# Performance work log

Measured on AMD Instinct MI355X. Metric: run time of the kernel, lower is better.

Reference implementation:

```python
import jax, jax.numpy as jnp
import numpy as np
import math

B, L, N, DIM, H = 2, 8, 1024, 512, 8
DH = DIM // H

def setup_inputs() -> dict:
    key = jax.random.key(0)
    ks = jax.random.split(key, 9)
    s = 1.0 / math.sqrt(DIM)
    return {
        "x": jax.random.normal(ks[0], (B, L, N, DIM), dtype=jnp.float32),
        "Wq": jax.random.normal(ks[1], (DIM, DIM), dtype=jnp.float32) * s,
        "bq": jnp.zeros((DIM,), dtype=jnp.float32),
        "Wk": jax.random.normal(ks[2], (DIM, DIM), dtype=jnp.float32) * s,
        "bk": jnp.zeros((DIM,), dtype=jnp.float32),
        "Wv": jax.random.normal(ks[3], (DIM, DIM), dtype=jnp.float32) * s,
        "bv": jnp.zeros((DIM,), dtype=jnp.float32),
        "Wo": jax.random.normal(ks[4], (DIM, DIM), dtype=jnp.float32) * s,
        "bo": jnp.zeros((DIM,), dtype=jnp.float32),
    }

def _split_heads(t):
    # 'b l n (h d) -> b l h n d'
    b, l, n, _ = t.shape
    return t.reshape(b, l, n, H, DH).transpose(0, 1, 3, 2, 4)

def reference(x, Wq, bq, Wk, bk, Wv, bv, Wo, bo):
    q = _split_heads(x @ Wq.T + bq)
    # FAITHFUL BUG: source maps (q, v, k) -> (q_mat, k_mat, v_mat),
    # so the "keys" come from the v projection and "values" from the k projection.
    k_mat = _split_heads(x @ Wv.T + bv)
    v_mat = _split_heads(x @ Wk.T + bk)
    # scale is sqrt(Dh * num_heads) = sqrt(dim), as in the source
    scores = jnp.einsum('blhnd,blhmd->blhnm', q, k_mat) / math.sqrt(DIM)
    weights = jax.nn.softmax(scores, axis=-1)
    inter = jnp.einsum('blhnm,blhmd->blhnd', weights, v_mat)
    # 'b l h n d -> b l n (h d)'
    inter = inter.transpose(0, 1, 3, 2, 4).reshape(x.shape[0], x.shape[1], x.shape[2], DIM)
    return inter @ Wo.T + bo
```

## Files before the change

### kernel.cpp

```cpp
#include <hip/hip_runtime.h>
#include <stdint.h>

#define DIMC 512
#define NSEQ 1024
#define BLT  16
#define NHEAD 8
#define DHD  64
#define MTOT (BLT*NSEQ)

typedef float f32x4 __attribute__((ext_vector_type(4)));
typedef short s16x8 __attribute__((ext_vector_type(8)));
typedef short s16x4 __attribute__((ext_vector_type(4)));

__device__ __forceinline__ unsigned short f2bf(float f) {
    unsigned int u = __float_as_uint(f);
    u += 0x7fffu + ((u >> 16) & 1u);
    return (unsigned short)(u >> 16);
}
__device__ __forceinline__ float bf2f(unsigned short h) {
    return __uint_as_float(((unsigned int)h) << 16);
}

#define QSCALE (0.04419417382415922f * 1.4426950408889634f)

__device__ __forceinline__ void gll16(const void* g, void* l) {
    __builtin_amdgcn_global_load_lds(
        (const __attribute__((address_space(1))) void*)g,
        (__attribute__((address_space(3))) void*)l, 16, 0, 0);
}

__device__ __forceinline__ f32x4 mfma16_bf16(s16x4 a, s16x4 b, f32x4 c) {
#if __has_builtin(__builtin_amdgcn_mfma_f32_16x16x16bf16_1k)
    return __builtin_amdgcn_mfma_f32_16x16x16bf16_1k(a, b, c, 0, 0, 0);
#else
    asm volatile("v_mfma_f32_16x16x16_bf16 %0, %1, %2, %0"
                 : "+v"(c) : "v"(a), "v"(b));
    return c;
#endif
}

__device__ __forceinline__ s16x4 pack_bf16x4(float p0, float p1, float p2, float p3) {
    union { unsigned int u[2]; s16x4 v; } pk;
    asm("v_cvt_pk_bf16_f32 %0, %1, %2" : "=v"(pk.u[0]) : "v"(p0), "v"(p1));
    asm("v_cvt_pk_bf16_f32 %0, %1, %2" : "=v"(pk.u[1]) : "v"(p2), "v"(p3));
    return pk.v;
}

__device__ __forceinline__ bool detect_bf16(const unsigned short* x) {
    int t = threadIdx.x & 63;
    unsigned short v = x[2 * t];
    int e = (v >> 7) & 0xFF;
    unsigned long long ball = __ballot(e < 100 || e > 137);
    return __popcll(ball) < 16;
}

struct ConvArgs {
    const void* src[9];
    unsigned short* dst[9];
};

__global__ __launch_bounds__(256) void conv_kernel(ConvArgs a,
                                                   const unsigned short* __restrict__ xdet) {
    const bool isbf = detect_bf16(xdet);
    int b = blockIdx.x;
    int seg, idx;
    if (b < 4096)      { seg = 0; idx = (b * 256 + threadIdx.x) * 8; }
    else if (b < 4608) { int t = b - 4096; seg = 1 + (t >> 7);
                         idx = (((t & 127) * 256) + threadIdx.x) * 8; }
    else               { int i = threadIdx.x * 8; seg = 5 + (i >> 9); idx = i & 511; }
    const void* s = a.src[seg];
    unsigned short* d = a.dst[seg];
    if (isbf) {
        *(uint4*)(d + idx) = *(const uint4*)((const unsigned short*)s + idx);
    } else {
        float4 t0 = *(const float4*)((const float*)s + idx);
        float4 t1 = *(const float4*)((const float*)s + idx + 4);
        ushort4 v0{f2bf(t0.x), f2bf(t0.y), f2bf(t0.z), f2bf(t0.w)};
        ushort4 v1{f2bf(t1.x), f2bf(t1.y), f2bf(t1.z), f2bf(t1.w)};
        *(ushort4*)(d + idx)     = v0;
        *(ushort4*)(d + idx + 4) = v1;
    }
}

__device__ __forceinline__ void gemm_core_async(
    const unsigned short* __restrict__ Ap, const unsigned short* __restrict__ Wp,
    int mBase, int nBase, unsigned short* Al, unsigned short* Bl, f32x4 acc[4][4])
{
    const int wave = threadIdx.x >> 6;
    const int lane = threadIdx.x & 63;
    const int lr = lane & 15, lg = lane >> 4;
    const int wm = wave >> 1, wn = wave & 1;
    const int srow = lane >> 3;
    const int scol = (lane & 7) * 8;

    #pragma unroll
    for (int a = 0; a < 4; ++a)
        #pragma unroll
        for (int b = 0; b < 4; ++b) acc[a][b] = (f32x4){0.f, 0.f, 0.f, 0.f};

    for (int k0 = 0; k0 < DIMC; k0 += 64) {
        #pragma unroll
        for (int i = 0; i < 4; ++i) {
            int rbase = (wave * 4 + i) * 8;
            gll16(Ap + (long)(mBase + rbase + srow) * DIMC + k0 + scol, Al + rbase * 64);
            gll16(Wp + (long)(nBase + rbase + srow) * DIMC + k0 + scol, Bl + rbase * 64);
        }
        __syncthreads();

        #pragma unroll
        for (int kk = 0; kk < 64; kk += 32) {
            s16x8 af[4], bf_[4];
            #pragma unroll
            for (int a = 0; a < 4; ++a)
                af[a] = *(const s16x8*)&Al[(wm * 64 + a * 16 + lr) * 64 + kk + lg * 8];
            #pragma unroll
            for (int b = 0; b < 4; ++b)
                bf_[b] = *(const s16x8*)&Bl[(wn * 64 + b * 16 + lr) * 64 + kk + lg * 8];
            #pragma unroll
            for (int a = 0; a < 4; ++a)
                #pragma unroll
                for (int b = 0; b < 4; ++b)
                    acc[a][b] = __builtin_amdgcn_mfma_f32_16x16x32_bf16(af[a], bf_[b], acc[a][b], 0, 0, 0);
        }
        __syncthreads();
    }
}

__global__ __launch_bounds__(256) void proj_kernel(
    const unsigned short* __restrict__ xb,
    const unsigned short* __restrict__ Wqb, const unsigned short* __restrict__ Wkb,
    const unsigned short* __restrict__ Wvb,
    const unsigned short* __restrict__ bqb, const unsigned short* __restrict__ bkb,
    const unsigned short* __restrict__ bvb,
    unsigned short* __restrict__ Q, unsigned short* __restrict__ K,
    unsigned short* __restrict__ Vt)
{
    const int z = blockIdx.z;
    const unsigned short* Wp = (z == 0) ? Wqb : ((z == 1) ? Wvb : Wkb);
    const unsigned short* bp = (z == 0) ? bqb : ((z == 1) ? bvb : bkb);
    unsigned short* outp = (z == 0) ? Q : ((z == 1) ? K : Vt);
    const float oscale = (z == 0) ? QSCALE : 1.0f;

    const int mBase = blockIdx.x * 128;
    const int nBase = blockIdx.y * 128;
    const int lane = threadIdx.x & 63;
    const int lr = lane & 15, lg = lane >> 4;
    const int wm = (threadIdx.x >> 6) >> 1, wn = (threadIdx.x >> 6) & 1;

    __shared__ unsigned short Al[128 * 64];
    __shared__ unsigned short Bl[128 * 64];
    f32x4 acc[4][4];
    gemm_core_async(xb, Wp, mBase, nBase, Al, Bl, acc);

    #pragma unroll
    for (int b = 0; b < 4; ++b) {
        int j = nBase + wn * 64 + b * 16 + lr;
        float bb = bf2f(bp[j]);
        int h = j >> 6, d = j & 63;
        #pragma unroll
        for (int a = 0; a < 4; ++a) {
            int m0 = mBase + wm * 64 + a * 16 + lg * 4;
            int bl = m0 >> 10, n0 = m0 & 1023;
            if (z == 2) {
                ushort4 pk;
                unsigned short* p = (unsigned short*)&pk;
                #pragma unroll
                for (int r = 0; r < 4; ++r) p[r] = f2bf(acc[a][b][r] + bb);
                *(ushort4*)&outp[(((bl << 3) + h) << 16) + (d << 10) + n0] = pk;
            } else {
                #pragma unroll
                for (int r = 0; r < 4; ++r) {
                    float v = (acc[a][b][r] + bb) * oscale;
                    outp[(((bl << 3) + h) << 16) + ((n0 + r) << 6) + d] = f2bf(v);
                }
            }
        }
    }
}

__global__ __launch_bounds__(256) void out_gemm_kernel(
    const unsigned short* __restrict__ inter, const unsigned short* __restrict__ Wob,
    const unsigned short* __restrict__ bob, void* __restrict__ outp,
    const unsigned short* __restrict__ xdet)
{
    const bool isbf = detect_bf16(xdet);
    const int mBase = blockIdx.x * 128;
    const int nBase = blockIdx.y * 128;
    const int lane = threadIdx.x & 63;
    const int lr = lane & 15, lg = lane >> 4;
    const int wm = (threadIdx.x >> 6) >> 1, wn = (threadIdx.x >> 6) & 1;

    __shared__ unsigned short Al[128 * 64];
    __shared__ unsigned short Bl[128 * 64];
    f32x4 acc[4][4];
    gemm_core_async(inter, Wob, mBase, nBase, Al, Bl, acc);

    #pragma unroll
    for (int b = 0; b < 4; ++b) {
        int j = nBase + wn * 64 + b * 16 + lr;
        float bb = bf2f(bob[j]);
        #pragma unroll
        for (int a = 0; a < 4; ++a) {
            #pragma unroll
            for (int r = 0; r < 4; ++r) {
                long m = mBase + wm * 64 + a * 16 + lg * 4 + r;
                float v = acc[a][b][r] + bb;
                if (isbf) ((unsigned short*)outp)[m * DIMC + j] = f2bf(v);
                else      ((float*)outp)[m * DIMC + j] = v;
            }
        }
    }
}

#define SWZ(row, col) ((row) * 64 + ((col) ^ (((row) & 7) * 8)))

__global__ __launch_bounds__(256, 3) void attn_kernel(
    const unsigned short* __restrict__ Q, const unsigned short* __restrict__ K,
    const unsigned short* __restrict__ Vt, unsigned short* __restrict__ inter)
{
    const int b = blockIdx.x;
    const int bh = b & 127;
    const int qt = b >> 7;
    const int tid = threadIdx.x;
    const int wave = tid >> 6;
    const int lane = tid & 63;
    const int lr = lane & 15;
    const int lg = lane >> 4;

    const unsigned short* Qb = Q + (long)bh * (NSEQ * DHD);
    const int qbase = qt * 128 + wave * 32;

    s16x8 qf[2][2];
    #pragma unroll
    for (int g = 0; g < 2; ++g)
        #pragma unroll
        for (int kk = 0; kk < 2; ++kk)
            qf[g][kk] = *(const s16x8*)&Qb[(qbase + g * 16 + lr) * DHD + kk * 32 + lg * 8];

    __shared__ unsigned short Kl[2][64 * 64];
    __shared__ unsigned short Vl[2][64 * 64];

    const int srow = tid >> 3;
    const int scol = ((tid & 7) * 8) ^ ((srow & 7) * 8);
    const unsigned short* kp = K  + (long)bh * (NSEQ * DHD) + srow * DHD  + scol;
    const unsigned short* vp = Vt + (long)bh * (NSEQ * DHD) + srow * NSEQ + scol;

    auto stage = [&](int buf, long ko, long vo) {
        unsigned short* Kb_ = &Kl[buf][0];
        unsigned short* Vb_ = &Vl[buf][0];
        gll16(kp + ko,         Kb_ + wave * 512);
        gll16(kp + ko + 2048,  Kb_ + wave * 512 + 2048);
        gll16(vp + vo,         Vb_ + wave * 512);
        gll16(vp + vo + 32768, Vb_ + wave * 512 + 2048);
    };

    f32x4 o[2][4];
    f32x4 lacc[2];
    #pragma unroll
    for (int g = 0; g < 2; ++g) {
        lacc[g] = (f32x4){0.f, 0.f, 0.f, 0.f};
        #pragma unroll
        for (int m = 0; m < 4; ++m) o[g][m] = (f32x4){0.f, 0.f, 0.f, 0.f};
    }
    const s16x4 onesf = {(short)0x3F80, (short)0x3F80, (short)0x3F80, (short)0x3F80};

    stage(0, 0, 0);
    __syncthreads();

    #pragma unroll 2
    for (int kt = 0; kt < 16; ++kt) {
        const int cur = kt & 1;
        if (kt < 15)
            stage(cur ^ 1, (long)(kt + 1) * (64 * DHD), (long)(kt + 1) * 64);

        const unsigned short* Kc = &Kl[cur][0];
        const unsigned short* Vc = &Vl[cur][0];

        f32x4 s[2][4];
        #pragma unroll
        for (int g = 0; g < 2; ++g)
            #pragma unroll
            for (int c = 0; c < 4; ++c) s[g][c] = (f32x4){0.f, 0.f, 0.f, 0.f};
        #pragma unroll
        for (int kk = 0; kk < 2; ++kk) {
            s16x8 af[4];
            #pragma unroll
            for (int c = 0; c < 4; ++c)
                af[c] = *(const s16x8*)&Kc[SWZ(c * 16 + lr, kk * 32 + lg * 8)];
            __builtin_amdgcn_s_setprio(1);
            #pragma unroll
            for (int g = 0; g < 2; ++g)
                #pragma unroll
                for (int c = 0; c < 4; ++c)
                    s[g][c] = __builtin_amdgcn_mfma_f32_16x16x32_bf16(af[c], qf[g][kk], s[g][c], 0, 0, 0);
            __builtin_amdgcn_s_setprio(0);
        }

        #pragma unroll
        for (int c = 0; c < 4; ++c) {
            s16x4 pb[2];
            #pragma unroll
            for (int g = 0; g < 2; ++g) {
                float p0 = __builtin_exp2f(s[g][c][0]);
                float p1 = __builtin_exp2f(s[g][c][1]);
                float p2 = __builtin_exp2f(s[g][c][2]);
                float p3 = __builtin_exp2f(s[g][c][3]);
                pb[g] = pack_bf16x4(p0, p1, p2, p3);
            }
            s16x4 va[4];
            #pragma unroll
            for (int m = 0; m < 4; ++m)
                va[m] = *(const s16x4*)&Vc[SWZ(m * 16 + lr, c * 16 + lg * 4)];
            __builtin_amdgcn_s_setprio(1);
            #pragma unroll
            for (int g = 0; g < 2; ++g) {
                lacc[g] = mfma16_bf16(onesf, pb[g], lacc[g]);
                #pragma unroll
                for (int m = 0; m < 4; ++m)
                    o[g][m] = mfma16_bf16(va[m], pb[g], o[g][m]);
            }
            __builtin_amdgcn_s_setprio(0);
        }

        if (kt < 15) __syncthreads();
    }

    const int bl = bh >> 3, h = bh & 7;
    #pragma unroll
    for (int g = 0; g < 2; ++g) {
        float inv = 1.f / lacc[g][0];
        const int n = qbase + g * 16 + lr;
        #pragma unroll
        for (int m = 0; m < 4; ++m) {
            ushort4 pk;
            unsigned short* p = (unsigned short*)&pk;
            #pragma unroll
            for (int r = 0; r < 4; ++r) p[r] = f2bf(o[g][m][r] * inv);
            *(ushort4*)&inter[((long)(bl * NSEQ + n)) * DIMC + h * 64 + m * 16 + lg * 4] = pk;
        }
    }
}

extern "C" void kernel_launch(void* const* d_in, const int* in_sizes, int n_in,
                              void* d_out, int out_size, void* d_ws, size_t ws_size,
                              hipStream_t stream) {
    const void* x  = d_in[0];
    const void* Wq = d_in[1]; const void* bq = d_in[2];
    const void* Wk = d_in[3]; const void* bk = d_in[4];
    const void* Wv = d_in[5]; const void* bv = d_in[6];
    const void* Wo = d_in[7]; const void* bo = d_in[8];

    char* ws = (char*)d_ws;
    unsigned short* xb  = (unsigned short*)ws;
    unsigned short* Q   = xb + (long)MTOT * DIMC;
    unsigned short* K   = Q  + (long)MTOT * DIMC;
    unsigned short* Vt  = K  + (long)MTOT * DIMC;
    unsigned short* Wqb = Vt + (long)MTOT * DIMC;
    unsigned short* Wkb = Wqb + DIMC * DIMC;
    unsigned short* Wvb = Wkb + DIMC * DIMC;
    unsigned short* Wob = Wvb + DIMC * DIMC;
    unsigned short* bqb = Wob + DIMC * DIMC;
    unsigned short* bkb = bqb + DIMC;
    unsigned short* bvb = bkb + DIMC;
    unsigned short* bob = bvb + DIMC;

    ConvArgs ca;
    ca.src[0] = x;  ca.src[1] = Wq; ca.src[2] = Wk; ca.src[3] = Wv; ca.src[4] = Wo;
    ca.src[5] = bq; ca.src[6] = bk; ca.src[7] = bv; ca.src[8] = bo;
    ca.dst[0] = xb;  ca.dst[1] = Wqb; ca.dst[2] = Wkb; ca.dst[3] = Wvb; ca.dst[4] = Wob;
    ca.dst[5] = bqb; ca.dst[6] = bkb; ca.dst[7] = bvb; ca.dst[8] = bob;
    conv_kernel<<<4609, 256, 0, stream>>>(ca, (const unsigned short*)x);

    dim3 gp(MTOT / 128, DIMC / 128, 3);
    proj_kernel<<<gp, 256, 0, stream>>>(xb, Wqb, Wkb, Wvb, bqb, bkb, bvb, Q, K, Vt);

    attn_kernel<<<8 * 128, 256, 0, stream>>>(Q, K, Vt, xb );

    dim3 go(MTOT / 128, DIMC / 128);
    out_gemm_kernel<<<go, 256, 0, stream>>>(xb , Wob, bob, d_out,
                                            (const unsigned short*)x);
}
```

Baseline: 218.2 us.

## Switch attention kernel to 32x32x16 MFMA tiles with permlane32 swaps

Rewrites the attention inner loop to use 32x32x16 bf16 MFMA instructions in place of the 16x16 variants, for both QK^T and PV. The S accumulator is converted to bf16 and rearranged into the B-operand layout with v_permlane32_swap, so no LDS round trip is needed. This cuts the MFMA instruction count and the V fragment loads, and the row-sum is now taken from a single 32x32 accumulator. Register pressure rises with the 16-wide accumulators, and the output store layout changes to match the 32x32 tile.

```diff
diff --git a/kernel.cpp b/kernel.cpp
--- a/kernel.cpp
+++ b/kernel.cpp
@@ -9,6 +9,7 @@
 #define MTOT (BLT*NSEQ)
 
 typedef float f32x4 __attribute__((ext_vector_type(4)));
+typedef float f32x16 __attribute__((ext_vector_type(16)));
 typedef short s16x8 __attribute__((ext_vector_type(8)));
 typedef short s16x4 __attribute__((ext_vector_type(4)));
 
@@ -29,21 +30,14 @@
         (__attribute__((address_space(3))) void*)l, 16, 0, 0);
 }
 
-__device__ __forceinline__ f32x4 mfma16_bf16(s16x4 a, s16x4 b, f32x4 c) {
-#if __has_builtin(__builtin_amdgcn_mfma_f32_16x16x16bf16_1k)
-    return __builtin_amdgcn_mfma_f32_16x16x16bf16_1k(a, b, c, 0, 0, 0);
-#else
-    asm volatile("v_mfma_f32_16x16x16_bf16 %0, %1, %2, %0"
-                 : "+v"(c) : "v"(a), "v"(b));
-    return c;
-#endif
-}
-
-__device__ __forceinline__ s16x4 pack_bf16x4(float p0, float p1, float p2, float p3) {
-    union { unsigned int u[2]; s16x4 v; } pk;
-    asm("v_cvt_pk_bf16_f32 %0, %1, %2" : "=v"(pk.u[0]) : "v"(p0), "v"(p1));
-    asm("v_cvt_pk_bf16_f32 %0, %1, %2" : "=v"(pk.u[1]) : "v"(p2), "v"(p3));
-    return pk.v;
+__device__ __forceinline__ unsigned int cvtpk(float lo, float hi) {
+    unsigned int r;
+    asm("v_cvt_pk_bf16_f32 %0, %1, %2" : "=v"(r) : "v"(lo), "v"(hi));
+    return r;
+}
+
+__device__ __forceinline__ void pl32swap(unsigned int &a, unsigned int &b) {
+    asm volatile("v_permlane32_swap_b32 %0, %1" : "+v"(a), "+v"(b));
 }
 
 __device__ __forceinline__ bool detect_bf16(const unsigned short* x) {
@@ -224,18 +218,16 @@
     const int tid = threadIdx.x;
     const int wave = tid >> 6;
     const int lane = tid & 63;
-    const int lr = lane & 15;
-    const int lg = lane >> 4;
+    const int l31 = lane & 31;
+    const int hi = lane >> 5;
 
     const unsigned short* Qb = Q + (long)bh * (NSEQ * DHD);
     const int qbase = qt * 128 + wave * 32;
 
-    s16x8 qf[2][2];
-    #pragma unroll
-    for (int g = 0; g < 2; ++g)
-        #pragma unroll
-        for (int kk = 0; kk < 2; ++kk)
-            qf[g][kk] = *(const s16x8*)&Qb[(qbase + g * 16 + lr) * DHD + kk * 32 + lg * 8];
+    s16x8 qf[4];
+    #pragma unroll
+    for (int k16 = 0; k16 < 4; ++k16)
+        qf[k16] = *(const s16x8*)&Qb[(qbase + l31) * DHD + k16 * 16 + hi * 8];
 
     __shared__ unsigned short Kl[2][64 * 64];
     __shared__ unsigned short Vl[2][64 * 64];
@@ -254,15 +246,13 @@
         gll16(vp + vo + 32768, Vb_ + wave * 512 + 2048);
     };
 
-    f32x4 o[2][4];
-    f32x4 lacc[2];
-    #pragma unroll
-    for (int g = 0; g < 2; ++g) {
-        lacc[g] = (f32x4){0.f, 0.f, 0.f, 0.f};
-        #pragma unroll
-        for (int m = 0; m < 4; ++m) o[g][m] = (f32x4){0.f, 0.f, 0.f, 0.f};
-    }
-    const s16x4 onesf = {(short)0x3F80, (short)0x3F80, (short)0x3F80, (short)0x3F80};
+    f32x16 o[2];
+    f32x16 lacc;
+    f32x16 zero16;
+    #pragma unroll
+    for (int r = 0; r < 16; ++r) { o[0][r] = 0.f; o[1][r] = 0.f; lacc[r] = 0.f; zero16[r] = 0.f; }
+    const s16x8 ones8 = {(short)0x3F80, (short)0x3F80, (short)0x3F80, (short)0x3F80,
+                         (short)0x3F80, (short)0x3F80, (short)0x3F80, (short)0x3F80};
 
     stage(0, 0, 0);
     __syncthreads();
@@ -276,49 +266,55 @@
         const unsigned short* Kc = &Kl[cur][0];
         const unsigned short* Vc = &Vl[cur][0];
 
-        f32x4 s[2][4];
-        #pragma unroll
-        for (int g = 0; g < 2; ++g)
-            #pragma unroll
-            for (int c = 0; c < 4; ++c) s[g][c] = (f32x4){0.f, 0.f, 0.f, 0.f};
-        #pragma unroll
-        for (int kk = 0; kk < 2; ++kk) {
+        #pragma unroll
+        for (int kc = 0; kc < 2; ++kc) {
             s16x8 af[4];
             #pragma unroll
-            for (int c = 0; c < 4; ++c)
-                af[c] = *(const s16x8*)&Kc[SWZ(c * 16 + lr, kk * 32 + lg * 8)];
+            for (int k16 = 0; k16 < 4; ++k16)
+                af[k16] = *(const s16x8*)&Kc[SWZ(kc * 32 + l31, k16 * 16 + hi * 8)];
+            f32x16 s;
             __builtin_amdgcn_s_setprio(1);
-            #pragma unroll
-            for (int g = 0; g < 2; ++g)
-                #pragma unroll
-                for (int c = 0; c < 4; ++c)
-                    s[g][c] = __builtin_amdgcn_mfma_f32_16x16x32_bf16(af[c], qf[g][kk], s[g][c], 0, 0, 0);
+            s = __builtin_amdgcn_mfma_f32_32x32x16_bf16(af[0], qf[0], zero16, 0, 0, 0);
+            s = __builtin_amdgcn_mfma_f32_32x32x16_bf16(af[1], qf[1], s, 0, 0, 0);
+            s = __builtin_amdgcn_mfma_f32_32x32x16_bf16(af[2], qf[2], s, 0, 0, 0);
+            s = __builtin_amdgcn_mfma_f32_32x32x16_bf16(af[3], qf[3], s, 0, 0, 0);
             __builtin_amdgcn_s_setprio(0);
-        }
-
-        #pragma unroll
-        for (int c = 0; c < 4; ++c) {
-            s16x4 pb[2];
-            #pragma unroll
-            for (int g = 0; g < 2; ++g) {
-                float p0 = __builtin_exp2f(s[g][c][0]);
-                float p1 = __builtin_exp2f(s[g][c][1]);
-                float p2 = __builtin_exp2f(s[g][c][2]);
-                float p3 = __builtin_exp2f(s[g][c][3]);
-                pb[g] = pack_bf16x4(p0, p1, p2, p3);
+
+            float p[16];
+            #pragma unroll
+            for (int r = 0; r < 16; ++r) p[r] = __builtin_exp2f(s[r]);
+            unsigned int w[4][2];
+            #pragma unroll
+            for (int b4 = 0; b4 < 4; ++b4) {
+                w[b4][0] = cvtpk(p[4 * b4 + 0], p[4 * b4 + 1]);
+                w[b4][1] = cvtpk(p[4 * b4 + 2], p[4 * b4 + 3]);
             }
-            s16x4 va[4];
-            #pragma unroll
-            for (int m = 0; m < 4; ++m)
-                va[m] = *(const s16x4*)&Vc[SWZ(m * 16 + lr, c * 16 + lg * 4)];
+            s16x8 frag[2];
+            #pragma unroll
+            for (int t16 = 0; t16 < 2; ++t16) {
+                unsigned int a0 = w[2 * t16][0], b0 = w[2 * t16 + 1][0];
+                unsigned int a1 = w[2 * t16][1], b1 = w[2 * t16 + 1][1];
+                pl32swap(a0, b0);
+                pl32swap(a1, b1);
+                union { unsigned int u[4]; s16x8 v; } f;
+                f.u[0] = a0; f.u[1] = a1; f.u[2] = b0; f.u[3] = b1;
+                frag[t16] = f.v;
+            }
+
+            s16x8 va[2][2];
+            #pragma unroll
+            for (int dt = 0; dt < 2; ++dt)
+                #pragma unroll
+                for (int t16 = 0; t16 < 2; ++t16)
+                    va[dt][t16] = *(const s16x8*)&Vc[SWZ(dt * 32 + l31, kc * 32 + t16 * 16 + hi * 8)];
             __builtin_amdgcn_s_setprio(1);
-            #pragma unroll
-            for (int g = 0; g < 2; ++g) {
-                lacc[g] = mfma16_bf16(onesf, pb[g], lacc[g]);
-                #pragma unroll
-                for (int m = 0; m < 4; ++m)
-                    o[g][m] = mfma16_bf16(va[m], pb[g], o[g][m]);
-            }
+            lacc = __builtin_amdgcn_mfma_f32_32x32x16_bf16(ones8, frag[0], lacc, 0, 0, 0);
+            lacc = __builtin_amdgcn_mfma_f32_32x32x16_bf16(ones8, frag[1], lacc, 0, 0, 0);
+            #pragma unroll
+            for (int dt = 0; dt < 2; ++dt)
+                #pragma unroll
+                for (int t16 = 0; t16 < 2; ++t16)
+                    o[dt] = __builtin_amdgcn_mfma_f32_32x32x16_bf16(va[dt][t16], frag[t16], o[dt], 0, 0, 0);
             __builtin_amdgcn_s_setprio(0);
         }
 
@@ -326,17 +322,17 @@
     }
 
     const int bl = bh >> 3, h = bh & 7;
-    #pragma unroll
-    for (int g = 0; g < 2; ++g) {
-        float inv = 1.f / lacc[g][0];
-        const int n = qbase + g * 16 + lr;
-        #pragma unroll
-        for (int m = 0; m < 4; ++m) {
-            ushort4 pk;
-            unsigned short* p = (unsigned short*)&pk;
-            #pragma unroll
-            for (int r = 0; r < 4; ++r) p[r] = f2bf(o[g][m][r] * inv);
-            *(ushort4*)&inter[((long)(bl * NSEQ + n)) * DIMC + h * 64 + m * 16 + lg * 4] = pk;
+    const int q = qbase + l31;
+    float inv = 1.f / lacc[0];
+    #pragma unroll
+    for (int dt = 0; dt < 2; ++dt) {
+        #pragma unroll
+        for (int b4 = 0; b4 < 4; ++b4) {
+            unsigned int w0 = cvtpk(o[dt][4 * b4 + 0] * inv, o[dt][4 * b4 + 1] * inv);
+            unsigned int w1 = cvtpk(o[dt][4 * b4 + 2] * inv, o[dt][4 * b4 + 3] * inv);
+            union { unsigned int u[2]; ushort4 v; } pk;
+            pk.u[0] = w0; pk.u[1] = w1;
+            *(ushort4*)&inter[((long)(bl * NSEQ + q)) * DIMC + h * 64 + dt * 32 + 8 * b4 + 4 * hi] = pk.v;
         }
     }
 }
```

Measured after the change: 219.3 us. About the same (+0.5%).
